# Optimization experiments

Hardware: AMD Instinct MI355X
Metric: run time of the kernel (lower is better)

The kernel has to match this reference:

```python
import jax, jax.numpy as jnp
import numpy as np

N = 4096
IN_DIM = 128
OUT_DIM = 64
LEAKY_SLOPE = 0.2


def setup_inputs() -> dict:
    key = jax.random.key(0)
    ks = jax.random.split(key, 8)
    H = jax.random.normal(ks[0], (N, IN_DIM), dtype=jnp.float32)
    # dense 0/1 adjacency per relation (int constants w.r.t. autodiff)
    A_buys = jax.random.randint(ks[1], (N, N), 0, 2, dtype=jnp.int32)
    A_views = jax.random.randint(ks[2], (N, N), 0, 2, dtype=jnp.int32)
    # xavier_uniform for W (stored [in, out]; Wh = H @ W == torch Linear with weight W.T)
    s_w = float(np.sqrt(6.0 / (IN_DIM + OUT_DIM)))
    W_buys = jax.random.uniform(ks[3], (IN_DIM, OUT_DIM), jnp.float32, -s_w, s_w)
    W_views = jax.random.uniform(ks[4], (IN_DIM, OUT_DIM), jnp.float32, -s_w, s_w)
    # xavier_uniform on a.view(1, 2*out_dim)
    s_a = float(np.sqrt(6.0 / (1 + 2 * OUT_DIM)))
    a_buys = jax.random.uniform(ks[5], (2 * OUT_DIM,), jnp.float32, -s_a, s_a)
    a_views = jax.random.uniform(ks[6], (2 * OUT_DIM,), jnp.float32, -s_a, s_a)
    bias = jnp.zeros((OUT_DIM,), dtype=jnp.float32)
    return {"H": H, "A_buys": A_buys, "A_views": A_views,
            "W_buys": W_buys, "W_views": W_views,
            "a_buys": a_buys, "a_views": a_views, "bias": bias}


def _relation(H, A, W, a):
    Wh = H @ W                                  # [N, OUT]
    # (cat(Wh_i, Wh_j) * a).sum(-1) == Wh_i @ a[:OUT] + Wh_j @ a[OUT:]
    s_i = Wh @ a[:OUT_DIM]                      # [N]
    s_j = Wh @ a[OUT_DIM:]                      # [N]
    e = jax.nn.leaky_relu(s_i[:, None] + s_j[None, :], LEAKY_SLOPE)  # [N, N]
    e = jnp.where(A == 0, -jnp.inf, e)
    alpha = jnp.nan_to_num(jax.nn.softmax(e, axis=1))                # isolated rows -> 0
    return alpha @ Wh                           # [N, OUT]


def reference(H, A_buys, A_views, W_buys, W_views, a_buys, a_views, bias):
    agg = _relation(H, A_buys, W_buys, a_buys) + _relation(H, A_views, W_views, a_views)
    return agg + bias
```

## Files before the change

### kernel.cpp

```cpp
#include <hip/hip_runtime.h>

#define NN 4096
#define IND 128
#define OUTD 64
#define LOG2E 1.44269504088896340736f

typedef __attribute__((ext_vector_type(4))) float  floatx4;
typedef __attribute__((ext_vector_type(8))) __bf16 bf16x8;
typedef __attribute__((ext_vector_type(2))) unsigned long long u64x2;

#if __has_builtin(__builtin_amdgcn_exp2f)
#define EXP2(x) __builtin_amdgcn_exp2f(x)
#else
#define EXP2(x) exp2f(x)
#endif

__device__ __forceinline__ unsigned short f2bf(float f) {
  unsigned int u = __float_as_uint(f);
  u += 0x7fffu + ((u >> 16) & 1u);
  return (unsigned short)(u >> 16);
}

__global__ __launch_bounds__(256) void gat_pack(
    const int* __restrict__ A0, const int* __restrict__ A1,
    unsigned long long* __restrict__ bits)
{
  const int t    = threadIdx.x;
  const int lane = t & 63;
  const int wv   = t >> 6;
  const int unit = blockIdx.x * 4 + wv;
  const int q    = unit & 3;
  const int i    = (unit >> 2) & (NN - 1);
  const int rel  = unit >> 14;
  const int* __restrict__ A = (rel ? A1 : A0) + (size_t)i * NN + q * 1024 + lane;

  unsigned long long wbuf[16];
#pragma unroll
  for (int k = 0; k < 16; k++)
    wbuf[k] = __ballot(A[k * 64] != 0);

  if (lane == 0) {
    u64x2* dst = (u64x2*)(bits + ((size_t)rel * NN + i) * 64 + q * 16);
#pragma unroll
    for (int k = 0; k < 8; k++) {
      u64x2 v; v[0] = wbuf[2 * k]; v[1] = wbuf[2 * k + 1];
      dst[k] = v;
    }
  }
}

__global__ __launch_bounds__(256) void gat_prep(
    const float* __restrict__ H,
    const float* __restrict__ W0, const float* __restrict__ W1,
    const float* __restrict__ av0, const float* __restrict__ av1,
    unsigned short* __restrict__ whT,
    float* __restrict__ sA,
    float* __restrict__ sB)
{
  const int rel = blockIdx.y;
  const float* __restrict__ W  = rel ? W1 : W0;
  const float* __restrict__ av = rel ? av1 : av0;
  const int i0 = blockIdx.x * 16;
  const int t = threadIdx.x;
  const int c = t & 63;
  const int wv = __builtin_amdgcn_readfirstlane(t >> 6);
  const float* __restrict__ hp = H + (size_t)(i0 + wv * 4) * IND;

  float acc0 = 0.f, acc1 = 0.f, acc2 = 0.f, acc3 = 0.f;
#pragma unroll 8
  for (int k = 0; k < IND; k += 4) {
    float4 h0 = *(const float4*)(hp + k);
    float4 h1 = *(const float4*)(hp + IND + k);
    float4 h2 = *(const float4*)(hp + 2 * IND + k);
    float4 h3 = *(const float4*)(hp + 3 * IND + k);
    float w0 = W[(k + 0) * OUTD + c];
    float w1 = W[(k + 1) * OUTD + c];
    float w2 = W[(k + 2) * OUTD + c];
    float w3 = W[(k + 3) * OUTD + c];
    acc0 += h0.x * w0 + h0.y * w1 + h0.z * w2 + h0.w * w3;
    acc1 += h1.x * w0 + h1.y * w1 + h1.z * w2 + h1.w * w3;
    acc2 += h2.x * w0 + h2.y * w1 + h2.z * w2 + h2.w * w3;
    acc3 += h3.x * w0 + h3.y * w1 + h3.z * w2 + h3.w * w3;
  }

  const float alo = av[c] * LOG2E, ahi = av[OUTD + c] * LOG2E;
  float pa0 = acc0 * alo, pa1 = acc1 * alo, pa2 = acc2 * alo, pa3 = acc3 * alo;
  float pb0 = acc0 * ahi, pb1 = acc1 * ahi, pb2 = acc2 * ahi, pb3 = acc3 * ahi;
#pragma unroll
  for (int off = 32; off >= 1; off >>= 1) {
    pa0 += __shfl_xor(pa0, off); pa1 += __shfl_xor(pa1, off);
    pa2 += __shfl_xor(pa2, off); pa3 += __shfl_xor(pa3, off);
    pb0 += __shfl_xor(pb0, off); pb1 += __shfl_xor(pb1, off);
    pb2 += __shfl_xor(pb2, off); pb3 += __shfl_xor(pb3, off);
  }
  const int ibase = i0 + wv * 4;
  if (c == 0) {
    float* sa = sA + rel * NN + ibase;
    float* sb = sB + rel * NN + ibase;
    sa[0] = pa0; sa[1] = pa1; sa[2] = pa2; sa[3] = pa3;
    sb[0] = pb0; sb[1] = pb1; sb[2] = pb2; sb[3] = pb3;
  }

  unsigned long long packed =
      (unsigned long long)f2bf(acc0)        | ((unsigned long long)f2bf(acc1) << 16) |
      ((unsigned long long)f2bf(acc2) << 32) | ((unsigned long long)f2bf(acc3) << 48);
  *(unsigned long long*)(whT + (size_t)(rel * OUTD + c) * NN + ibase) = packed;
}

__global__ __launch_bounds__(512) void gat_main(
    const unsigned long long* __restrict__ bits,
    const unsigned short* __restrict__ whT,
    const float* __restrict__ sA, const float* __restrict__ sB,
    float* __restrict__ numer,
    float* __restrict__ denom,
    int ns)
{
  __shared__ float red[8][1024];
  __shared__ float dred[8][16];
  const int rel  = blockIdx.y;
  const int sp   = blockIdx.z;
  const int i0   = blockIdx.x * 16;
  const int t    = threadIdx.x;
  const int w    = t >> 6;
  const int lane = t & 63;
  const int m    = lane & 15;
  const int quad = lane >> 4;
  const int i    = i0 + m;
  const float si = sA[rel * NN + i];
  const float* __restrict__ sb = sB + rel * NN;
  const unsigned short* __restrict__ wh = whT + (size_t)rel * OUTD * NN;
  const unsigned long long* __restrict__ bp = bits + ((size_t)rel * NN + i) * 64;

  const int jwin = NN / (ns * 8);
  const int jw0  = sp * (NN / ns) + w * jwin;
  const int nch  = jwin >> 8;

  floatx4 acc0 = {0.f, 0.f, 0.f, 0.f}, acc1 = acc0, acc2 = acc0, acc3 = acc0;
  float dsum = 0.f;

  for (int c2 = 0; c2 < nch; c2++) {
    const int jc = jw0 + c2 * 256;
    u64x2 bA = *(const u64x2*)(bp + (jc >> 6));
    u64x2 bB = *(const u64x2*)(bp + (jc >> 6) + 2);
    const float*          psb = sb + jc + quad * 8;
    const unsigned short* pb0 = wh + (size_t)(0 * 16 + m) * NN + jc + quad * 8;
    const unsigned short* pb1 = wh + (size_t)(1 * 16 + m) * NN + jc + quad * 8;
    const unsigned short* pb2 = wh + (size_t)(2 * 16 + m) * NN + jc + quad * 8;
    const unsigned short* pb3 = wh + (size_t)(3 * 16 + m) * NN + jc + quad * 8;

#pragma unroll
    for (int jt = 0; jt < 256; jt += 32) {
      float4 s0 = *(const float4*)(psb + jt);
      float4 s1 = *(const float4*)(psb + jt + 4);
      bf16x8 b0 = *(const bf16x8*)(pb0 + jt);
      bf16x8 b1 = *(const bf16x8*)(pb1 + jt);
      bf16x8 b2 = *(const bf16x8*)(pb2 + jt);
      bf16x8 b3 = *(const bf16x8*)(pb3 + jt);

      const unsigned long long wbits =
          (jt < 64) ? bA[0] : (jt < 128) ? bA[1] : (jt < 192) ? bB[0] : bB[1];
      const unsigned bmask = (unsigned)(wbits >> ((jt & 63) + quad * 8)) & 0xFFu;

      float t0 = si + s0.x, t1 = si + s0.y, t2 = si + s0.z, t3 = si + s0.w;
      float t4 = si + s1.x, t5 = si + s1.y, t6 = si + s1.z, t7 = si + s1.w;
      float e0 = EXP2(fmaxf(t0, 0.2f * t0));
      float e1 = EXP2(fmaxf(t1, 0.2f * t1));
      float e2 = EXP2(fmaxf(t2, 0.2f * t2));
      float e3 = EXP2(fmaxf(t3, 0.2f * t3));
      float e4 = EXP2(fmaxf(t4, 0.2f * t4));
      float e5 = EXP2(fmaxf(t5, 0.2f * t5));
      float e6 = EXP2(fmaxf(t6, 0.2f * t6));
      float e7 = EXP2(fmaxf(t7, 0.2f * t7));
      e0 = (bmask & 1u)   ? e0 : 0.f;
      e1 = (bmask & 2u)   ? e1 : 0.f;
      e2 = (bmask & 4u)   ? e2 : 0.f;
      e3 = (bmask & 8u)   ? e3 : 0.f;
      e4 = (bmask & 16u)  ? e4 : 0.f;
      e5 = (bmask & 32u)  ? e5 : 0.f;
      e6 = (bmask & 64u)  ? e6 : 0.f;
      e7 = (bmask & 128u) ? e7 : 0.f;
      dsum += ((e0 + e1) + (e2 + e3)) + ((e4 + e5) + (e6 + e7));

      bf16x8 af;
      af[0] = (__bf16)e0; af[1] = (__bf16)e1; af[2] = (__bf16)e2; af[3] = (__bf16)e3;
      af[4] = (__bf16)e4; af[5] = (__bf16)e5; af[6] = (__bf16)e6; af[7] = (__bf16)e7;

      acc0 = __builtin_amdgcn_mfma_f32_16x16x32_bf16(af, b0, acc0, 0, 0, 0);
      acc1 = __builtin_amdgcn_mfma_f32_16x16x32_bf16(af, b1, acc1, 0, 0, 0);
      acc2 = __builtin_amdgcn_mfma_f32_16x16x32_bf16(af, b2, acc2, 0, 0, 0);
      acc3 = __builtin_amdgcn_mfma_f32_16x16x32_bf16(af, b3, acc3, 0, 0, 0);
    }
  }

  dsum += __shfl_xor(dsum, 16);
  dsum += __shfl_xor(dsum, 32);

#pragma unroll
  for (int r = 0; r < 4; r++) {
    const int row = quad * 4 + r;
    red[w][row * 64 + 0 * 16 + m] = acc0[r];
    red[w][row * 64 + 1 * 16 + m] = acc1[r];
    red[w][row * 64 + 2 * 16 + m] = acc2[r];
    red[w][row * 64 + 3 * 16 + m] = acc3[r];
  }
  if (lane < 16) dred[w][lane] = dsum;
  __syncthreads();

  const int c  = t & 63;
  const int r0 = t >> 6;
  const size_t base = ((size_t)rel * ns + sp) * NN;
#pragma unroll
  for (int rr = r0; rr < 16; rr += 8) {
    float nsum = 0.f, ds = 0.f;
#pragma unroll
    for (int ww = 0; ww < 8; ww++) { nsum += red[ww][rr * 64 + c]; ds += dred[ww][rr]; }
    numer[(base + i0 + rr) * OUTD + c] = nsum;
    if (c == 0) denom[base + i0 + rr] = ds;
  }
}

__global__ __launch_bounds__(256) void gat_combine(
    const float* __restrict__ numer, const float* __restrict__ denom,
    const float* __restrict__ bias, float* __restrict__ out, int ns)
{
  const int idx = blockIdx.x * 256 + threadIdx.x;
  const int i  = idx >> 4;
  const int c4 = idx & 15;
  const float4* nv = (const float4*)numer;

  float4 o = ((const float4*)bias)[c4];
#pragma unroll
  for (int rel = 0; rel < 2; rel++) {
    float4 n = {0.f, 0.f, 0.f, 0.f};
    float  d = 0.f;
    for (int s = 0; s < ns; s++) {
      const size_t base = ((size_t)rel * ns + s) * NN + i;
      float4 np = nv[base * 16 + c4];
      n.x += np.x; n.y += np.y; n.z += np.z; n.w += np.w;
      d += denom[base];
    }
    float inv = d > 0.f ? 1.f / d : 0.f;
    o.x += n.x * inv; o.y += n.y * inv; o.z += n.z * inv; o.w += n.w * inv;
  }
  ((float4*)out)[idx] = o;
}

extern "C" void kernel_launch(void* const* d_in, const int* in_sizes, int n_in,
                              void* d_out, int out_size, void* d_ws, size_t ws_size,
                              hipStream_t stream) {
  const float* H    = (const float*)d_in[0];
  const int*   A0   = (const int*)d_in[1];
  const int*   A1   = (const int*)d_in[2];
  const float* W0   = (const float*)d_in[3];
  const float* W1   = (const float*)d_in[4];
  const float* av0  = (const float*)d_in[5];
  const float* av1  = (const float*)d_in[6];
  const float* bias = (const float*)d_in[7];
  float* out = (float*)d_out;

  const size_t whT_b = (size_t)2 * OUTD * NN * 2;
  const size_t s_b   = (size_t)2 * NN * 4;
  const size_t bit_b = (size_t)2 * NN * 64 * 8;
  const size_t need2 = whT_b + 2 * s_b + bit_b + (size_t)2 * 2 * NN * OUTD * 4 + (size_t)2 * 2 * NN * 4;
  const int ns = (ws_size >= need2) ? 2 : 1;

  unsigned short*     whT  = (unsigned short*)d_ws;
  float*              sA   = (float*)((char*)d_ws + whT_b);
  float*              sB   = (float*)((char*)d_ws + whT_b + s_b);
  unsigned long long* bits = (unsigned long long*)((char*)d_ws + whT_b + 2 * s_b);
  float*              numer = (float*)((char*)d_ws + whT_b + 2 * s_b + bit_b);
  float*              denom = numer + (size_t)2 * ns * NN * OUTD;

  gat_pack<<<8192, 256, 0, stream>>>(A0, A1, bits);
  gat_prep<<<dim3(NN / 16, 2), 256, 0, stream>>>(H, W0, W1, av0, av1, whT, sA, sB);
  gat_main<<<dim3(NN / 16, 2, ns), 512, 0, stream>>>(bits, whT, sA, sB, numer, denom, ns);
  gat_combine<<<(NN * OUTD / 4) / 256, 256, 0, stream>>>(numer, denom, bias, out, ns);
}
```

Baseline: 214.0 us.

## Fuse adjacency bit-packing into main attention kernel with LDS-staged MFMA operands

Drops the separate pass that packs the int32 adjacency into bitmasks. The main kernel now reads A directly with coalesced int4 loads, computes the masked exp weights, writes them as bf16 into a swizzled per-wave LDS slice, and feeds them to MFMA. Wh is stored in a blocked layout so the B-operand loads are contiguous. The row sum is computed by an extra MFMA against a vector of ones instead of a scalar accumulation. This removes one kernel launch and the bitmask round trip through memory, at the cost of more LDS traffic and a larger LDS footprint per block.

```diff
diff --git a/kernel.cpp b/kernel.cpp
--- a/kernel.cpp
+++ b/kernel.cpp
@@ -7,7 +7,6 @@
 
 typedef __attribute__((ext_vector_type(4))) float  floatx4;
 typedef __attribute__((ext_vector_type(8))) __bf16 bf16x8;
-typedef __attribute__((ext_vector_type(2))) unsigned long long u64x2;
 
 #if __has_builtin(__builtin_amdgcn_exp2f)
 #define EXP2(x) __builtin_amdgcn_exp2f(x)
@@ -21,41 +20,12 @@
   return (unsigned short)(u >> 16);
 }
 
-__global__ __launch_bounds__(256) void gat_pack(
-    const int* __restrict__ A0, const int* __restrict__ A1,
-    unsigned long long* __restrict__ bits)
-{
-  const int t    = threadIdx.x;
-  const int lane = t & 63;
-  const int wv   = t >> 6;
-  const int unit = blockIdx.x * 4 + wv;
-  const int q    = unit & 3;
-  const int i    = (unit >> 2) & (NN - 1);
-  const int rel  = unit >> 14;
-  const int* __restrict__ A = (rel ? A1 : A0) + (size_t)i * NN + q * 1024 + lane;
-
-  unsigned long long wbuf[16];
-#pragma unroll
-  for (int k = 0; k < 16; k++)
-    wbuf[k] = __ballot(A[k * 64] != 0);
-
-  if (lane == 0) {
-    u64x2* dst = (u64x2*)(bits + ((size_t)rel * NN + i) * 64 + q * 16);
-#pragma unroll
-    for (int k = 0; k < 8; k++) {
-      u64x2 v; v[0] = wbuf[2 * k]; v[1] = wbuf[2 * k + 1];
-      dst[k] = v;
-    }
-  }
-}
-
 __global__ __launch_bounds__(256) void gat_prep(
     const float* __restrict__ H,
     const float* __restrict__ W0, const float* __restrict__ W1,
     const float* __restrict__ av0, const float* __restrict__ av1,
-    unsigned short* __restrict__ whT,
-    float* __restrict__ sA,
-    float* __restrict__ sB)
+    unsigned short* __restrict__ whF,
+    float* __restrict__ sA, float* __restrict__ sB)
 {
   const int rel = blockIdx.y;
   const float* __restrict__ W  = rel ? W1 : W0;
@@ -104,106 +74,104 @@
   unsigned long long packed =
       (unsigned long long)f2bf(acc0)        | ((unsigned long long)f2bf(acc1) << 16) |
       ((unsigned long long)f2bf(acc2) << 32) | ((unsigned long long)f2bf(acc3) << 48);
-  *(unsigned long long*)(whT + (size_t)(rel * OUTD + c) * NN + ibase) = packed;
-}
-
-__global__ __launch_bounds__(512) void gat_main(
-    const unsigned long long* __restrict__ bits,
-    const unsigned short* __restrict__ whT,
+  *(unsigned long long*)(whF + ((size_t)(rel * 512 + (ibase >> 3)) * 64 + c) * 8 + (ibase & 7)) = packed;
+}
+
+__global__ __launch_bounds__(512, 4) void gat_fused(
+    const int* __restrict__ A0, const int* __restrict__ A1,
+    const unsigned short* __restrict__ whF,
     const float* __restrict__ sA, const float* __restrict__ sB,
     float* __restrict__ numer,
     float* __restrict__ denom,
     int ns)
 {
-  __shared__ float red[8][1024];
-  __shared__ float dred[8][16];
+  __shared__ char lds[65536];
   const int rel  = blockIdx.y;
   const int sp   = blockIdx.z;
   const int i0   = blockIdx.x * 16;
   const int t    = threadIdx.x;
   const int w    = t >> 6;
   const int lane = t & 63;
+  const int quad = lane >> 4;
   const int m    = lane & 15;
-  const int quad = lane >> 4;
-  const int i    = i0 + m;
-  const float si = sA[rel * NN + i];
-  const float* __restrict__ sb = sB + rel * NN;
-  const unsigned short* __restrict__ wh = whT + (size_t)rel * OUTD * NN;
-  const unsigned long long* __restrict__ bp = bits + ((size_t)rel * NN + i) * 64;
-
-  const int jwin = NN / (ns * 8);
-  const int jw0  = sp * (NN / ns) + w * jwin;
-  const int nch  = jwin >> 8;
-
-  floatx4 acc0 = {0.f, 0.f, 0.f, 0.f}, acc1 = acc0, acc2 = acc0, acc3 = acc0;
-  float dsum = 0.f;
-
-  for (int c2 = 0; c2 < nch; c2++) {
-    const int jc = jw0 + c2 * 256;
-    u64x2 bA = *(const u64x2*)(bp + (jc >> 6));
-    u64x2 bB = *(const u64x2*)(bp + (jc >> 6) + 2);
-    const float*          psb = sb + jc + quad * 8;
-    const unsigned short* pb0 = wh + (size_t)(0 * 16 + m) * NN + jc + quad * 8;
-    const unsigned short* pb1 = wh + (size_t)(1 * 16 + m) * NN + jc + quad * 8;
-    const unsigned short* pb2 = wh + (size_t)(2 * 16 + m) * NN + jc + quad * 8;
-    const unsigned short* pb3 = wh + (size_t)(3 * 16 + m) * NN + jc + quad * 8;
-
-#pragma unroll
-    for (int jt = 0; jt < 256; jt += 32) {
-      float4 s0 = *(const float4*)(psb + jt);
-      float4 s1 = *(const float4*)(psb + jt + 4);
-      bf16x8 b0 = *(const bf16x8*)(pb0 + jt);
-      bf16x8 b1 = *(const bf16x8*)(pb1 + jt);
-      bf16x8 b2 = *(const bf16x8*)(pb2 + jt);
-      bf16x8 b3 = *(const bf16x8*)(pb3 + jt);
-
-      const unsigned long long wbits =
-          (jt < 64) ? bA[0] : (jt < 128) ? bA[1] : (jt < 192) ? bB[0] : bB[1];
-      const unsigned bmask = (unsigned)(wbits >> ((jt & 63) + quad * 8)) & 0xFFu;
-
-      float t0 = si + s0.x, t1 = si + s0.y, t2 = si + s0.z, t3 = si + s0.w;
-      float t4 = si + s1.x, t5 = si + s1.y, t6 = si + s1.z, t7 = si + s1.w;
-      float e0 = EXP2(fmaxf(t0, 0.2f * t0));
-      float e1 = EXP2(fmaxf(t1, 0.2f * t1));
-      float e2 = EXP2(fmaxf(t2, 0.2f * t2));
-      float e3 = EXP2(fmaxf(t3, 0.2f * t3));
-      float e4 = EXP2(fmaxf(t4, 0.2f * t4));
-      float e5 = EXP2(fmaxf(t5, 0.2f * t5));
-      float e6 = EXP2(fmaxf(t6, 0.2f * t6));
-      float e7 = EXP2(fmaxf(t7, 0.2f * t7));
-      e0 = (bmask & 1u)   ? e0 : 0.f;
-      e1 = (bmask & 2u)   ? e1 : 0.f;
-      e2 = (bmask & 4u)   ? e2 : 0.f;
-      e3 = (bmask & 8u)   ? e3 : 0.f;
-      e4 = (bmask & 16u)  ? e4 : 0.f;
-      e5 = (bmask & 32u)  ? e5 : 0.f;
-      e6 = (bmask & 64u)  ? e6 : 0.f;
-      e7 = (bmask & 128u) ? e7 : 0.f;
-      dsum += ((e0 + e1) + (e2 + e3)) + ((e4 + e5) + (e6 + e7));
-
-      bf16x8 af;
-      af[0] = (__bf16)e0; af[1] = (__bf16)e1; af[2] = (__bf16)e2; af[3] = (__bf16)e3;
-      af[4] = (__bf16)e4; af[5] = (__bf16)e5; af[6] = (__bf16)e6; af[7] = (__bf16)e7;
-
-      acc0 = __builtin_amdgcn_mfma_f32_16x16x32_bf16(af, b0, acc0, 0, 0, 0);
-      acc1 = __builtin_amdgcn_mfma_f32_16x16x32_bf16(af, b1, acc1, 0, 0, 0);
-      acc2 = __builtin_amdgcn_mfma_f32_16x16x32_bf16(af, b2, acc2, 0, 0, 0);
-      acc3 = __builtin_amdgcn_mfma_f32_16x16x32_bf16(af, b3, acc3, 0, 0, 0);
-    }
-  }
-
-  dsum += __shfl_xor(dsum, 16);
-  dsum += __shfl_xor(dsum, 32);
-
+  const int* __restrict__ A = rel ? A1 : A0;
+  const unsigned short* __restrict__ wh = whF + (size_t)rel * 512 * 64 * 8;
+  const float* __restrict__ sbp = sB + rel * NN;
+
+  char* slice = lds + w * 8192;
+  const int ql    = (lane >> 1) & 3;
+  const int wbase = (lane >> 3) * 1024 + ql * 256 + (lane & 1) * 8;
+  const int rbase = (quad * 16 + (m ^ quad)) * 16;
+
+  const float siv = sA[rel * NN + i0 + m];
+
+  floatx4 acc0 = {0.f,0.f,0.f,0.f}, acc1 = acc0, acc2 = acc0, acc3 = acc0, acc4 = acc0;
+  bf16x8 vone;
+#pragma unroll
+  for (int k = 0; k < 8; k++) vone[k] = (__bf16)1.0f;
+
+  const int nwin = (ns == 2) ? 1 : 2;
+  for (int win = 0; win < nwin; win++) {
+    const int jw = sp * (NN / ns) + (w * nwin + win) * 256;
+    float4 sjv = *(const float4*)(sbp + jw + lane * 4);
+
+#pragma unroll
+    for (int half = 0; half < 2; half++) {
+      int4 av[8];
+      const int* pA = A + (size_t)(i0 + half * 8) * NN + jw + lane * 4;
+#pragma unroll
+      for (int r = 0; r < 8; r++) av[r] = *(const int4*)(pA + (size_t)r * NN);
+#pragma unroll
+      for (int r = 0; r < 8; r++) {
+        const int rr = half * 8 + r;
+        const float si = __uint_as_float(__builtin_amdgcn_readlane(__float_as_uint(siv), rr));
+        float t0 = si + sjv.x, t1 = si + sjv.y, t2 = si + sjv.z, t3 = si + sjv.w;
+        float e0 = EXP2(fmaxf(t0, 0.2f * t0));
+        float e1 = EXP2(fmaxf(t1, 0.2f * t1));
+        float e2 = EXP2(fmaxf(t2, 0.2f * t2));
+        float e3 = EXP2(fmaxf(t3, 0.2f * t3));
+        e0 = av[r].x ? e0 : 0.f;
+        e1 = av[r].y ? e1 : 0.f;
+        e2 = av[r].z ? e2 : 0.f;
+        e3 = av[r].w ? e3 : 0.f;
+        uint2 pk;
+        pk.x = (unsigned)f2bf(e0) | ((unsigned)f2bf(e1) << 16);
+        pk.y = (unsigned)f2bf(e2) | ((unsigned)f2bf(e3) << 16);
+        *(uint2*)(slice + wbase + ((rr ^ ql) << 4)) = pk;
+      }
+    }
+
+    const unsigned short* bb = wh + (size_t)(jw >> 3) * 512 + (size_t)m * 8;
+#pragma unroll
+    for (int ks = 0; ks < 8; ks++) {
+      bf16x8 a = *(const bf16x8*)(slice + ks * 1024 + rbase);
+      const unsigned short* bq = bb + (size_t)(ks * 4 + quad) * 512;
+      bf16x8 b0 = *(const bf16x8*)(bq + 0 * 128);
+      bf16x8 b1 = *(const bf16x8*)(bq + 1 * 128);
+      bf16x8 b2 = *(const bf16x8*)(bq + 2 * 128);
+      bf16x8 b3 = *(const bf16x8*)(bq + 3 * 128);
+      acc0 = __builtin_amdgcn_mfma_f32_16x16x32_bf16(a, b0, acc0, 0, 0, 0);
+      acc1 = __builtin_amdgcn_mfma_f32_16x16x32_bf16(a, b1, acc1, 0, 0, 0);
+      acc2 = __builtin_amdgcn_mfma_f32_16x16x32_bf16(a, b2, acc2, 0, 0, 0);
+      acc3 = __builtin_amdgcn_mfma_f32_16x16x32_bf16(a, b3, acc3, 0, 0, 0);
+      acc4 = __builtin_amdgcn_mfma_f32_16x16x32_bf16(a, vone, acc4, 0, 0, 0);
+    }
+  }
+
+  float* redw  = (float*)slice;
+  float* dredw = (float*)(slice + 4096);
 #pragma unroll
   for (int r = 0; r < 4; r++) {
     const int row = quad * 4 + r;
-    red[w][row * 64 + 0 * 16 + m] = acc0[r];
-    red[w][row * 64 + 1 * 16 + m] = acc1[r];
-    red[w][row * 64 + 2 * 16 + m] = acc2[r];
-    red[w][row * 64 + 3 * 16 + m] = acc3[r];
-  }
-  if (lane < 16) dred[w][lane] = dsum;
+    redw[row * 64 + 0 * 16 + m] = acc0[r];
+    redw[row * 64 + 1 * 16 + m] = acc1[r];
+    redw[row * 64 + 2 * 16 + m] = acc2[r];
+    redw[row * 64 + 3 * 16 + m] = acc3[r];
+  }
+  if (m == 0) {
+#pragma unroll
+    for (int r = 0; r < 4; r++) dredw[quad * 4 + r] = acc4[r];
+  }
   __syncthreads();
 
   const int c  = t & 63;
@@ -213,7 +181,10 @@
   for (int rr = r0; rr < 16; rr += 8) {
     float nsum = 0.f, ds = 0.f;
 #pragma unroll
-    for (int ww = 0; ww < 8; ww++) { nsum += red[ww][rr * 64 + c]; ds += dred[ww][rr]; }
+    for (int ww = 0; ww < 8; ww++) {
+      nsum += ((const float*)(lds + ww * 8192))[rr * 64 + c];
+      ds   += ((const float*)(lds + ww * 8192 + 4096))[rr];
+    }
     numer[(base + i0 + rr) * OUTD + c] = nsum;
     if (c == 0) denom[base + i0 + rr] = ds;
   }
@@ -258,21 +229,18 @@
   const float* bias = (const float*)d_in[7];
   float* out = (float*)d_out;
 
-  const size_t whT_b = (size_t)2 * OUTD * NN * 2;
+  const size_t whF_b = (size_t)2 * 512 * 64 * 8 * 2;
   const size_t s_b   = (size_t)2 * NN * 4;
-  const size_t bit_b = (size_t)2 * NN * 64 * 8;
-  const size_t need2 = whT_b + 2 * s_b + bit_b + (size_t)2 * 2 * NN * OUTD * 4 + (size_t)2 * 2 * NN * 4;
+  const size_t need2 = whF_b + 2 * s_b + (size_t)2 * 2 * NN * OUTD * 4 + (size_t)2 * 2 * NN * 4;
   const int ns = (ws_size >= need2) ? 2 : 1;
 
-  unsigned short*     whT  = (unsigned short*)d_ws;
-  float*              sA   = (float*)((char*)d_ws + whT_b);
-  float*              sB   = (float*)((char*)d_ws + whT_b + s_b);
-  unsigned long long* bits = (unsigned long long*)((char*)d_ws + whT_b + 2 * s_b);
-  float*              numer = (float*)((char*)d_ws + whT_b + 2 * s_b + bit_b);
-  float*              denom = numer + (size_t)2 * ns * NN * OUTD;
-
-  gat_pack<<<8192, 256, 0, stream>>>(A0, A1, bits);
-  gat_prep<<<dim3(NN / 16, 2), 256, 0, stream>>>(H, W0, W1, av0, av1, whT, sA, sB);
-  gat_main<<<dim3(NN / 16, 2, ns), 512, 0, stream>>>(bits, whT, sA, sB, numer, denom, ns);
+  unsigned short* whF   = (unsigned short*)d_ws;
+  float*          sA    = (float*)((char*)d_ws + whF_b);
+  float*          sB    = (float*)((char*)d_ws + whF_b + s_b);
+  float*          numer = (float*)((char*)d_ws + whF_b + 2 * s_b);
+  float*          denom = numer + (size_t)2 * ns * NN * OUTD;
+
+  gat_prep<<<dim3(NN / 16, 2), 256, 0, stream>>>(H, W0, W1, av0, av1, whF, sA, sB);
+  gat_fused<<<dim3(NN / 16, 2, ns), 512, 0, stream>>>(A0, A1, whF, sA, sB, numer, denom, ns);
   gat_combine<<<(NN * OUTD / 4) / 256, 256, 0, stream>>>(numer, denom, bias, out, ns);
 }
```

New measurement: 187.8 us. -12.2%, faster.
